# Optimization experiments

Hardware: AMD Instinct MI355X
Metric: run time of the kernel (lower is better)

Reference implementation:

```python
import jax, jax.numpy as jnp
import numpy as np

B, T, H, V = 64, 512, 300, 50257


def setup_inputs() -> dict:
    key = jax.random.key(0)
    k0, k1, k2, k3, k4 = jax.random.split(key, 5)
    tokens = jax.random.randint(k0, (B, T), 0, V, dtype=jnp.int32)
    ihs = jnp.zeros((B, H), jnp.float32)
    emb = jax.random.normal(k1, (V, H), jnp.float32) * 0.02
    W = jax.random.normal(k2, (H, H), jnp.float32) * (1.0 / np.sqrt(H))
    U = jax.random.normal(k3, (H, H), jnp.float32) * (1.0 / np.sqrt(H))
    Wout = jax.random.normal(k4, (V, H), jnp.float32) * 0.02
    bout = jnp.zeros((V,), jnp.float32)
    return {"ihs": ihs, "tokens": tokens, "emb": emb, "W": W, "U": U,
            "Wout": Wout, "bout": bout}


def reference(ihs, tokens, emb, W, U, Wout, bout):
    # Embedding lookup: [B, T, H]
    x = emb[tokens]
    # Precompute input projection for all timesteps: U x_t (Linear: x @ U^T)
    ux = jnp.einsum('bth,gh->btg', x, U)  # [B, T, H]
    ux_tmajor = jnp.swapaxes(ux, 0, 1)    # [T, B, H]

    def step(h, ux_t):
        # h_t = tanh(W h_{t-1} + U x_t)
        h_next = jnp.tanh(h @ W.T + ux_t)
        return h_next, h_next

    h_last, _ = jax.lax.scan(step, ihs, ux_tmajor)
    # final hidden state -> vocab logits
    logits = h_last @ Wout.T + bout  # [B, V]
    return logits
```

## Files before the change

kernel.cpp:

```cpp
#include <hip/hip_runtime.h>
#include <math.h>

#define H 300
#define BB 64
#define TT 512
#define VV 50257
#define KC 30

__global__ void transpose_k(const float* __restrict__ in, float* __restrict__ out) {
    int idx = blockIdx.x * blockDim.x + threadIdx.x;
    if (idx < H * H) {
        int r = idx / H, c = idx - r * H;
        out[idx] = in[c * H + r];
    }
}

__global__ __launch_bounds__(256) void ux_k(const int* __restrict__ tokens,
                                            const float* __restrict__ emb,
                                            const float* __restrict__ Ut,
                                            float* __restrict__ ux) {
    __shared__ __align__(16) float x_s[KC][BB];
    __shared__ __align__(16) float ut_s[KC][304];
    __shared__ int tok_s[BB];

    const int t = blockIdx.x;
    const int tid = threadIdx.x;
    if (tid < BB) tok_s[tid] = tokens[tid * TT + t];

    const int tb = tid >> 4;
    const int tg = tid & 15;
    const int b0 = tb * 4;
    const int g0 = tg * 20;
    const bool active = (tg < 15);

    float acc[4][20];
#pragma unroll
    for (int i = 0; i < 4; ++i)
#pragma unroll
        for (int j = 0; j < 20; ++j) acc[i][j] = 0.f;

    __syncthreads();

    for (int h0 = 0; h0 < H; h0 += KC) {
        for (int i = tid; i < BB * 32; i += 256) {
            int b = i >> 5, k = i & 31;
            if (k < KC) x_s[k][b] = emb[tok_s[b] * H + h0 + k];
        }
        for (int i = tid; i < KC * H; i += 256) {
            int k = i / H, g = i - k * H;
            ut_s[k][g] = Ut[(h0 + k) * H + g];
        }
        __syncthreads();
        if (active) {
#pragma unroll 2
            for (int k = 0; k < KC; ++k) {
                float4 xa = *reinterpret_cast<const float4*>(&x_s[k][b0]);
                float4 u0 = *reinterpret_cast<const float4*>(&ut_s[k][g0 + 0]);
                float4 u1 = *reinterpret_cast<const float4*>(&ut_s[k][g0 + 4]);
                float4 u2 = *reinterpret_cast<const float4*>(&ut_s[k][g0 + 8]);
                float4 u3 = *reinterpret_cast<const float4*>(&ut_s[k][g0 + 12]);
                float4 u4 = *reinterpret_cast<const float4*>(&ut_s[k][g0 + 16]);
                const float xr[4] = {xa.x, xa.y, xa.z, xa.w};
                const float ur[20] = {u0.x, u0.y, u0.z, u0.w,
                                      u1.x, u1.y, u1.z, u1.w,
                                      u2.x, u2.y, u2.z, u2.w,
                                      u3.x, u3.y, u3.z, u3.w,
                                      u4.x, u4.y, u4.z, u4.w};
#pragma unroll
                for (int i = 0; i < 4; ++i)
#pragma unroll
                    for (int j = 0; j < 20; ++j)
                        acc[i][j] += xr[i] * ur[j];
            }
        }
        __syncthreads();
    }

    if (active) {
#pragma unroll
        for (int i = 0; i < 4; ++i) {
            float* dst = ux + (t * BB + b0 + i) * H + g0;
#pragma unroll
            for (int jq = 0; jq < 5; ++jq) {
                *reinterpret_cast<float4*>(dst + jq * 4) =
                    make_float4(acc[i][jq * 4 + 0], acc[i][jq * 4 + 1],
                                acc[i][jq * 4 + 2], acc[i][jq * 4 + 3]);
            }
        }
    }
}

#define RNN_Q15(X) X(0) X(1) X(2) X(3) X(4) X(5) X(6) X(7) X(8) X(9) \
    X(10) X(11) X(12) X(13) X(14)

__global__ __attribute__((amdgpu_flat_work_group_size(512, 512), amdgpu_waves_per_eu(2, 2)))
void rnn_k(const float* __restrict__ W,
           const float* __restrict__ ux,
           const float* __restrict__ ihs,
           float* __restrict__ hlast) {
    __shared__ __align__(16) float shpool[20800];
    float* h_s = shpool;
    float* p_s = shpool + 304;

    const int b = blockIdx.x;
    const int tid = threadIdx.x;
    const int tt = (tid < 500) ? tid : 499;
    const int c  = tt / 100;
    const int g3 = tt - c * 100;

    const float4* w0p = reinterpret_cast<const float4*>(W + (size_t)(g3      ) * H + c * 60);
    const float4* w1p = reinterpret_cast<const float4*>(W + (size_t)(g3 + 100) * H + c * 60);
    const float4* w2p = reinterpret_cast<const float4*>(W + (size_t)(g3 + 200) * H + c * 60);

#define RNN_DW(q) float4 w0_##q = w0p[q]; float4 w1_##q = w1p[q]; float4 w2_##q = w2p[q];
    RNN_Q15(RNN_DW)
#undef RNN_DW

    if (tid < H) h_s[tid] = ihs[b * H + tid];

    const float* uxb = ux + (size_t)b * H;
    float u0 = 0.f, u1 = 0.f, u2 = 0.f;
    if (tid < 100) {
        u0 = uxb[g3];
        u1 = uxb[100 + g3];
        u2 = uxb[200 + g3];
    }
    __syncthreads();

    const float4* hs4 = reinterpret_cast<const float4*>(h_s);
    const int c15 = c * 15;

#pragma unroll 1
    for (int t = 0; t < TT; ++t) {
        float n0 = 0.f, n1 = 0.f, n2 = 0.f;
        if (tid < 100 && t + 1 < TT) {
            const float* nx = uxb + (size_t)(t + 1) * (BB * H);
            n0 = nx[g3];
            n1 = nx[100 + g3];
            n2 = nx[200 + g3];
        }
        float4 a0 = make_float4(0.f, 0.f, 0.f, 0.f);
        float4 a1 = make_float4(0.f, 0.f, 0.f, 0.f);
        float4 a2 = make_float4(0.f, 0.f, 0.f, 0.f);
#define RNN_FMA(q) { float4 h4 = hs4[c15 + q]; \
        a0.x += w0_##q.x * h4.x; a0.y += w0_##q.y * h4.y; \
        a0.z += w0_##q.z * h4.z; a0.w += w0_##q.w * h4.w; \
        a1.x += w1_##q.x * h4.x; a1.y += w1_##q.y * h4.y; \
        a1.z += w1_##q.z * h4.z; a1.w += w1_##q.w * h4.w; \
        a2.x += w2_##q.x * h4.x; a2.y += w2_##q.y * h4.y; \
        a2.z += w2_##q.z * h4.z; a2.w += w2_##q.w * h4.w; }
        RNN_Q15(RNN_FMA)
#undef RNN_FMA
        float pA0 = (a0.x + a0.y) + (a0.z + a0.w);
        float pA1 = (a1.x + a1.y) + (a1.z + a1.w);
        float pA2 = (a2.x + a2.y) + (a2.z + a2.w);
        if (tid < 500 && c != 0) {
            p_s[(c - 1) * 304 + g3      ] = pA0;
            p_s[(c - 1) * 304 + g3 + 100] = pA1;
            p_s[(c - 1) * 304 + g3 + 200] = pA2;
        }
        __syncthreads();
        if (tid < 100) {
            float z0 = pA0 + u0;
            float z1 = pA1 + u1;
            float z2 = pA2 + u2;
#pragma unroll
            for (int j = 0; j < 4; ++j) {
                z0 += p_s[j * 304 + g3];
                z1 += p_s[j * 304 + g3 + 100];
                z2 += p_s[j * 304 + g3 + 200];
            }
            float e0 = __expf(2.f * z0);
            float e1 = __expf(2.f * z1);
            float e2 = __expf(2.f * z2);
            h_s[g3      ] = 1.f - 2.f * __builtin_amdgcn_rcpf(e0 + 1.f);
            h_s[g3 + 100] = 1.f - 2.f * __builtin_amdgcn_rcpf(e1 + 1.f);
            h_s[g3 + 200] = 1.f - 2.f * __builtin_amdgcn_rcpf(e2 + 1.f);
        }
        u0 = n0; u1 = n1; u2 = n2;
        __syncthreads();
    }
    if (tid < H) hlast[b * H + tid] = h_s[tid];
}

__global__ __launch_bounds__(256) void logits_k(const float* __restrict__ hlast,
                                                const float* __restrict__ Wout,
                                                const float* __restrict__ bout,
                                                float* __restrict__ out) {
    __shared__ __align__(16) float Ws[32 * 132];
    __shared__ __align__(16) float hs[32 * 76];
    const int tid = threadIdx.x;
    const int tv = tid & 31;
    const int tb = tid >> 5;
    const int v0 = blockIdx.x * 128;

    float acc[8][4];
#pragma unroll
    for (int i = 0; i < 8; ++i)
#pragma unroll
        for (int j = 0; j < 4; ++j) acc[i][j] = 0.f;

    for (int hb = 0; hb < H; hb += 32) {
        __syncthreads();
        {
            const int vp = tid >> 1;
            const int hloc = (tid & 1) * 16;
            int vv = v0 + vp; if (vv > VV - 1) vv = VV - 1;
            const float* wrow = Wout + (size_t)vv * H + hb + hloc;
#pragma unroll
            for (int i = 0; i < 4; ++i) {
                const int hg = hb + hloc + i * 4;
                float4 val;
                if (hg + 3 < H) {
                    val = *reinterpret_cast<const float4*>(wrow + i * 4);
                } else {
                    val.x = (hg + 0 < H) ? wrow[i * 4 + 0] : 0.f;
                    val.y = (hg + 1 < H) ? wrow[i * 4 + 1] : 0.f;
                    val.z = (hg + 2 < H) ? wrow[i * 4 + 2] : 0.f;
                    val.w = (hg + 3 < H) ? wrow[i * 4 + 3] : 0.f;
                }
                Ws[(hloc + i * 4 + 0) * 132 + vp] = val.x;
                Ws[(hloc + i * 4 + 1) * 132 + vp] = val.y;
                Ws[(hloc + i * 4 + 2) * 132 + vp] = val.z;
                Ws[(hloc + i * 4 + 3) * 132 + vp] = val.w;
            }
        }
        {
            const int bb = tid >> 2;
            const int hl = (tid & 3) * 8;
            const float* hrow = hlast + bb * H + hb + hl;
#pragma unroll
            for (int i = 0; i < 2; ++i) {
                const int hg = hb + hl + i * 4;
                float4 val;
                if (hg + 3 < H) {
                    val = *reinterpret_cast<const float4*>(hrow + i * 4);
                } else {
                    val.x = (hg + 0 < H) ? hrow[i * 4 + 0] : 0.f;
                    val.y = (hg + 1 < H) ? hrow[i * 4 + 1] : 0.f;
                    val.z = (hg + 2 < H) ? hrow[i * 4 + 2] : 0.f;
                    val.w = (hg + 3 < H) ? hrow[i * 4 + 3] : 0.f;
                }
                hs[(hl + i * 4 + 0) * 76 + bb] = val.x;
                hs[(hl + i * 4 + 1) * 76 + bb] = val.y;
                hs[(hl + i * 4 + 2) * 76 + bb] = val.z;
                hs[(hl + i * 4 + 3) * 76 + bb] = val.w;
            }
        }
        __syncthreads();
        const float4* Ws4 = reinterpret_cast<const float4*>(Ws);
        const float4* hs4 = reinterpret_cast<const float4*>(hs);
#pragma unroll
        for (int h2 = 0; h2 < 32; ++h2) {
            float4 w4  = Ws4[h2 * 33 + tv];
            float4 h4a = hs4[h2 * 19 + tb * 2];
            float4 h4b = hs4[h2 * 19 + tb * 2 + 1];
            const float hv[8] = {h4a.x, h4a.y, h4a.z, h4a.w,
                                 h4b.x, h4b.y, h4b.z, h4b.w};
#pragma unroll
            for (int bi = 0; bi < 8; ++bi) {
                acc[bi][0] += hv[bi] * w4.x;
                acc[bi][1] += hv[bi] * w4.y;
                acc[bi][2] += hv[bi] * w4.z;
                acc[bi][3] += hv[bi] * w4.w;
            }
        }
    }

    const int vg = v0 + tv * 4;
    float4 bq;
    if (vg + 3 < VV) bq = *reinterpret_cast<const float4*>(bout + vg);
    else {
        bq.x = (vg + 0 < VV) ? bout[vg + 0] : 0.f;
        bq.y = (vg + 1 < VV) ? bout[vg + 1] : 0.f;
        bq.z = (vg + 2 < VV) ? bout[vg + 2] : 0.f;
        bq.w = (vg + 3 < VV) ? bout[vg + 3] : 0.f;
    }
#pragma unroll
    for (int bi = 0; bi < 8; ++bi) {
        const int bb = tb * 8 + bi;
        float* op = out + (size_t)bb * VV + vg;
        if (vg + 0 < VV) op[0] = acc[bi][0] + bq.x;
        if (vg + 1 < VV) op[1] = acc[bi][1] + bq.y;
        if (vg + 2 < VV) op[2] = acc[bi][2] + bq.z;
        if (vg + 3 < VV) op[3] = acc[bi][3] + bq.w;
    }
}

extern "C" void kernel_launch(void* const* d_in, const int* in_sizes, int n_in,
                              void* d_out, int out_size, void* d_ws, size_t ws_size,
                              hipStream_t stream) {
    const float* ihs    = (const float*)d_in[0];
    const int*   tokens = (const int*)  d_in[1];
    const float* emb    = (const float*)d_in[2];
    const float* W      = (const float*)d_in[3];
    const float* U      = (const float*)d_in[4];
    const float* Wout   = (const float*)d_in[5];
    const float* bout   = (const float*)d_in[6];
    float* out = (float*)d_out;

    char* ws = (char*)d_ws;
    float* Ut    = (float*)(ws + 0);
    float* hlast = (float*)(ws + 400000);
    float* ux    = (float*)(ws + 1048576);

    const int tp_blocks = (H * H + 255) / 256;
    transpose_k<<<tp_blocks, 256, 0, stream>>>(U, Ut);
    ux_k<<<TT, 256, 0, stream>>>(tokens, emb, Ut, ux);
    rnn_k<<<BB, 512, 0, stream>>>(W, ux, ihs, hlast);
    logits_k<<<(VV + 127) / 128, 256, 0, stream>>>(hlast, Wout, bout, out);
}
```

Baseline: 715.7 us.

## Widen RNN block to 768 threads, spread reduction and tanh across 300 threads

The recurrent kernel now uses 768 threads per batch row. Each thread holds two rows of W instead of three, and all five column-chunk partials go to shared memory. The final reduction and tanh are spread across 300 threads instead of 100 doing three outputs each. __syncthreads is replaced by an explicit lgkmcnt wait plus s_barrier with scheduling fences. The aim is to shorten the serial per-timestep critical path, at the cost of more waves joining each barrier and one extra partial write.

```diff
diff --git a/kernel.cpp b/kernel.cpp
--- a/kernel.cpp
+++ b/kernel.cpp
@@ -93,7 +93,14 @@
 #define RNN_Q15(X) X(0) X(1) X(2) X(3) X(4) X(5) X(6) X(7) X(8) X(9) \
     X(10) X(11) X(12) X(13) X(14)
 
-__global__ __attribute__((amdgpu_flat_work_group_size(512, 512), amdgpu_waves_per_eu(2, 2)))
+__device__ __forceinline__ void rnn_bar_lds() {
+    __builtin_amdgcn_sched_barrier(0);
+    asm volatile("s_waitcnt lgkmcnt(0)" ::: "memory");
+    __builtin_amdgcn_s_barrier();
+    __builtin_amdgcn_sched_barrier(0);
+}
+
+__global__ __attribute__((amdgpu_flat_work_group_size(768, 768), amdgpu_waves_per_eu(3, 3)))
 void rnn_k(const float* __restrict__ W,
            const float* __restrict__ ux,
            const float* __restrict__ ihs,
@@ -104,27 +111,22 @@
 
     const int b = blockIdx.x;
     const int tid = threadIdx.x;
-    const int tt = (tid < 500) ? tid : 499;
-    const int c  = tt / 100;
-    const int g3 = tt - c * 100;
-
-    const float4* w0p = reinterpret_cast<const float4*>(W + (size_t)(g3      ) * H + c * 60);
-    const float4* w1p = reinterpret_cast<const float4*>(W + (size_t)(g3 + 100) * H + c * 60);
-    const float4* w2p = reinterpret_cast<const float4*>(W + (size_t)(g3 + 200) * H + c * 60);
-
-#define RNN_DW(q) float4 w0_##q = w0p[q]; float4 w1_##q = w1p[q]; float4 w2_##q = w2p[q];
+    const int tt = (tid < 750) ? tid : 749;
+    const int c  = tt / 150;
+    const int g2 = tt - c * 150;
+
+    const float4* w0p = reinterpret_cast<const float4*>(W + (size_t)(g2      ) * H + c * 60);
+    const float4* w1p = reinterpret_cast<const float4*>(W + (size_t)(g2 + 150) * H + c * 60);
+
+#define RNN_DW(q) float4 w0_##q = w0p[q]; float4 w1_##q = w1p[q];
     RNN_Q15(RNN_DW)
 #undef RNN_DW
 
     if (tid < H) h_s[tid] = ihs[b * H + tid];
 
-    const float* uxb = ux + (size_t)b * H;
-    float u0 = 0.f, u1 = 0.f, u2 = 0.f;
-    if (tid < 100) {
-        u0 = uxb[g3];
-        u1 = uxb[100 + g3];
-        u2 = uxb[200 + g3];
-    }
+    const float* uxr = ux + (size_t)b * H + tid;
+    float u = 0.f;
+    if (tid < H) u = uxr[0];
     __syncthreads();
 
     const float4* hs4 = reinterpret_cast<const float4*>(h_s);
@@ -132,53 +134,36 @@
 
 #pragma unroll 1
     for (int t = 0; t < TT; ++t) {
-        float n0 = 0.f, n1 = 0.f, n2 = 0.f;
-        if (tid < 100 && t + 1 < TT) {
-            const float* nx = uxb + (size_t)(t + 1) * (BB * H);
-            n0 = nx[g3];
-            n1 = nx[100 + g3];
-            n2 = nx[200 + g3];
-        }
+        float n = 0.f;
+        if (tid < H && t + 1 < TT)
+            n = uxr[(size_t)(t + 1) * (BB * H)];
         float4 a0 = make_float4(0.f, 0.f, 0.f, 0.f);
         float4 a1 = make_float4(0.f, 0.f, 0.f, 0.f);
-        float4 a2 = make_float4(0.f, 0.f, 0.f, 0.f);
 #define RNN_FMA(q) { float4 h4 = hs4[c15 + q]; \
         a0.x += w0_##q.x * h4.x; a0.y += w0_##q.y * h4.y; \
         a0.z += w0_##q.z * h4.z; a0.w += w0_##q.w * h4.w; \
         a1.x += w1_##q.x * h4.x; a1.y += w1_##q.y * h4.y; \
-        a1.z += w1_##q.z * h4.z; a1.w += w1_##q.w * h4.w; \
-        a2.x += w2_##q.x * h4.x; a2.y += w2_##q.y * h4.y; \
-        a2.z += w2_##q.z * h4.z; a2.w += w2_##q.w * h4.w; }
+        a1.z += w1_##q.z * h4.z; a1.w += w1_##q.w * h4.w; }
         RNN_Q15(RNN_FMA)
 #undef RNN_FMA
-        float pA0 = (a0.x + a0.y) + (a0.z + a0.w);
-        float pA1 = (a1.x + a1.y) + (a1.z + a1.w);
-        float pA2 = (a2.x + a2.y) + (a2.z + a2.w);
-        if (tid < 500 && c != 0) {
-            p_s[(c - 1) * 304 + g3      ] = pA0;
-            p_s[(c - 1) * 304 + g3 + 100] = pA1;
-            p_s[(c - 1) * 304 + g3 + 200] = pA2;
-        }
-        __syncthreads();
-        if (tid < 100) {
-            float z0 = pA0 + u0;
-            float z1 = pA1 + u1;
-            float z2 = pA2 + u2;
-#pragma unroll
-            for (int j = 0; j < 4; ++j) {
-                z0 += p_s[j * 304 + g3];
-                z1 += p_s[j * 304 + g3 + 100];
-                z2 += p_s[j * 304 + g3 + 200];
-            }
-            float e0 = __expf(2.f * z0);
-            float e1 = __expf(2.f * z1);
-            float e2 = __expf(2.f * z2);
-            h_s[g3      ] = 1.f - 2.f * __builtin_amdgcn_rcpf(e0 + 1.f);
-            h_s[g3 + 100] = 1.f - 2.f * __builtin_amdgcn_rcpf(e1 + 1.f);
-            h_s[g3 + 200] = 1.f - 2.f * __builtin_amdgcn_rcpf(e2 + 1.f);
-        }
-        u0 = n0; u1 = n1; u2 = n2;
-        __syncthreads();
+        float pA = (a0.x + a0.y) + (a0.z + a0.w);
+        float pB = (a1.x + a1.y) + (a1.z + a1.w);
+        if (tid < 750) {
+            p_s[c * 304 + g2      ] = pA;
+            p_s[c * 304 + g2 + 150] = pB;
+        }
+        rnn_bar_lds();
+        if (tid < H) {
+            float z = p_s[tid] + u;
+            z += p_s[304 + tid];
+            z += p_s[608 + tid];
+            z += p_s[912 + tid];
+            z += p_s[1216 + tid];
+            float e = __expf(2.f * z);
+            h_s[tid] = 1.f - 2.f * __builtin_amdgcn_rcpf(e + 1.f);
+        }
+        u = n;
+        rnn_bar_lds();
     }
     if (tid < H) hlast[b * H + tid] = h_s[tid];
 }
@@ -307,6 +292,6 @@
     const int tp_blocks = (H * H + 255) / 256;
     transpose_k<<<tp_blocks, 256, 0, stream>>>(U, Ut);
     ux_k<<<TT, 256, 0, stream>>>(tokens, emb, Ut, ux);
-    rnn_k<<<BB, 512, 0, stream>>>(W, ux, ihs, hlast);
+    rnn_k<<<BB, 768, 0, stream>>>(W, ux, ihs, hlast);
     logits_k<<<(VV + 127) / 128, 256, 0, stream>>>(hlast, Wout, bout, out);
 }
```

After: 726.5 us. About the same (+1.5%).
